# Kernel tuning notes

Measured on AMD Instinct MI355X. Metric: run time of the kernel, lower is better.

Reference implementation:

```python
import jax, jax.numpy as jnp
import numpy as np

NUM_HEADS = 16
HEAD_DIM = 64
MIN_FREQ = 1.0
MAX_FREQ = 40.0


def _rope_cos_sin(t, dtype):
    # golden_gate RoPE, pos_dim=1: geometric frequency ladder in [min_freq, max_freq],
    # positions normalized to [0,1) so max_freq ~ highest spatial frequency.
    n = HEAD_DIM // 2
    j = jnp.arange(n, dtype=dtype)
    freqs = MIN_FREQ * (MAX_FREQ / MIN_FREQ) ** (j / (n - 1))  # [n]
    pos = jnp.arange(t, dtype=dtype) / t                        # [t]
    theta = 2.0 * jnp.pi * pos[:, None] * freqs[None, :]        # [t, n]
    return jnp.cos(theta), jnp.sin(theta)


def _apply_rope(x, cos, sin):
    # x: [b, h, t, d]; rotate-half convention
    n = HEAD_DIM // 2
    x1, x2 = x[..., :n], x[..., n:]
    return jnp.concatenate([x1 * cos - x2 * sin, x1 * sin + x2 * cos], axis=-1)


def setup_inputs() -> dict:
    key = jax.random.key(0)
    ks = jax.random.split(key, 5)
    b, t, c = 4, 2048, 1024
    s = 1.0 / np.sqrt(c)
    return {
        "x": jax.random.normal(ks[0], (b, t, c), dtype=jnp.float32),
        "qkv_w": jax.random.normal(ks[1], (3 * c, c), dtype=jnp.float32) * s,
        "qkv_b": jax.random.normal(ks[2], (3 * c,), dtype=jnp.float32) * 0.01,
        "proj_w": jax.random.normal(ks[3], (c, c), dtype=jnp.float32) * s,
        "proj_b": jax.random.normal(ks[4], (c,), dtype=jnp.float32) * 0.01,
    }


def reference(x, qkv_w, qkv_b, proj_w, proj_b):
    b, t, c = x.shape
    h, d = NUM_HEADS, HEAD_DIM
    qkv = x @ qkv_w.T + qkv_b                                   # [b, t, 3c]
    qkv = qkv.reshape(b, t, 3, h, d).transpose(0, 3, 1, 2, 4)   # [b, h, t, 3, d]
    q, k, v = qkv[..., 0, :], qkv[..., 1, :], qkv[..., 2, :]    # each [b, h, t, d]
    cos, sin = _rope_cos_sin(t, x.dtype)
    q = _apply_rope(q, cos, sin)
    k = _apply_rope(k, cos, sin)
    scale = 1.0 / jnp.sqrt(jnp.asarray(d, dtype=x.dtype))
    scores = jnp.einsum("bhqd,bhkd->bhqk", q, k) * scale        # [b, h, t, t]
    attn = jax.nn.softmax(scores, axis=-1)
    out = jnp.einsum("bhqk,bhkd->bhqd", attn, v)                # [b, h, t, d]
    out = out.transpose(0, 2, 1, 3).reshape(b, t, h * d)        # [b, t, c]
    return out @ proj_w.T + proj_b
```

## Files before the change

### kernel.cpp

```cpp
#include <hip/hip_runtime.h>

typedef unsigned short u16;
typedef unsigned int   u32;
typedef __attribute__((ext_vector_type(8))) short s16x8;
typedef __attribute__((ext_vector_type(4))) float f32x4;
typedef __attribute__((ext_vector_type(16))) float f32x16;

#define MFMA16(a, b, c) __builtin_amdgcn_mfma_f32_16x16x32_bf16((a), (b), (c), 0, 0, 0)
#define MFMA32(a, b, c) __builtin_amdgcn_mfma_f32_32x32x16_bf16((a), (b), (c), 0, 0, 0)
#define EXP2R(x) __builtin_amdgcn_exp2f(x)

#define GLD16(gp, lp) __builtin_amdgcn_global_load_lds(                     \
    (const __attribute__((address_space(1))) void*)(gp),                    \
    (__attribute__((address_space(3))) void*)(lp), 16, 0, 0)

#define PWOFF 1048576ull

__device__ __forceinline__ u16 f2b(float f) {
  union { float f; unsigned i; } x; x.f = f;
  unsigned r = x.i + 0x7FFFu + ((x.i >> 16) & 1u);
  return (u16)(r >> 16);
}
__device__ __forceinline__ u32 cvtpk_bf16(float a, float b) {
  u32 r;
  asm("v_cvt_pk_bf16_f32 %0, %1, %2" : "=v"(r) : "v"(a), "v"(b));
  return r;
}
__device__ __forceinline__ s16x8 cvt8(const float* __restrict__ p) {
  f32x4 a = *(const f32x4*)p;
  f32x4 b = *(const f32x4*)(p + 4);
  union { u32 u[4]; s16x8 v; } o;
  o.u[0] = cvtpk_bf16(a[0], a[1]);
  o.u[1] = cvtpk_bf16(a[2], a[3]);
  o.u[2] = cvtpk_bf16(b[0], b[1]);
  o.u[3] = cvtpk_bf16(b[2], b[3]);
  return o.v;
}

__device__ __forceinline__ void plswap(u32& a, u32& b) {
#if __has_builtin(__builtin_amdgcn_permlane32_swap)
  auto r = __builtin_amdgcn_permlane32_swap(a, b, false, false);
  a = r[0]; b = r[1];
#else
  asm volatile("v_permlane32_swap_b32 %0, %1" : "+v"(a), "+v"(b));
#endif
}
__device__ __forceinline__ float pair32(float x, int hi) {
  union { float f; u32 u; } a, b;
  a.f = x; b.f = x;
  plswap(a.u, b.u);
  return hi ? a.f : b.f;
}
__device__ __forceinline__ s16x8 mk_pa(float e0, float e1, float e2, float e3,
                                       float e4, float e5, float e6, float e7) {
  u32 a0 = cvtpk_bf16(e0, e1), b0 = cvtpk_bf16(e4, e5);
  u32 a1 = cvtpk_bf16(e2, e3), b1 = cvtpk_bf16(e6, e7);
  plswap(a0, b0);
  plswap(a1, b1);
  union { u32 u[4]; s16x8 v; } x;
  x.u[0] = a0; x.u[1] = a1; x.u[2] = b0; x.u[3] = b1;
  return x.v;
}

#define SM_GRP(sv, ofs, pa_out, ps_out) {                                  \
    float e0 = EXP2R((sv)[(ofs) + 0] * C - mC);                            \
    float e1 = EXP2R((sv)[(ofs) + 1] * C - mC);                            \
    float e2 = EXP2R((sv)[(ofs) + 2] * C - mC);                            \
    float e3 = EXP2R((sv)[(ofs) + 3] * C - mC);                            \
    float e4 = EXP2R((sv)[(ofs) + 4] * C - mC);                            \
    float e5 = EXP2R((sv)[(ofs) + 5] * C - mC);                            \
    float e6 = EXP2R((sv)[(ofs) + 6] * C - mC);                            \
    float e7 = EXP2R((sv)[(ofs) + 7] * C - mC);                            \
    (pa_out) = mk_pa(e0, e1, e2, e3, e4, e5, e6, e7);                      \
    (ps_out) = ((e0 + e1) + (e2 + e3)) + ((e4 + e5) + (e6 + e7));          \
  }

#define QKT_P(QF, KA, KB, S0, S1) {                                        \
    _Pragma("unroll")                                                      \
    for (int r = 0; r < 16; ++r) { (S0)[r] = 0.f; (S1)[r] = 0.f; }         \
    _Pragma("unroll")                                                      \
    for (int ks = 0; ks < 4; ++ks) {                                       \
      (S0) = MFMA32((KA)[ks], (QF)[ks], (S0));                             \
      (S1) = MFMA32((KB)[ks], (QF)[ks], (S1));                             \
    }                                                                      \
  }

#define SMAX_P(S0, S1, PA0, PA1, PA2, PA3, MR, LI, O0, O1) {               \
    float m8[8];                                                           \
    _Pragma("unroll")                                                      \
    for (int r = 0; r < 8; ++r)                                            \
      m8[r] = fmaxf(fmaxf((S0)[r], (S0)[r + 8]),                           \
                    fmaxf((S1)[r], (S1)[r + 8]));                          \
    float mx = fmaxf(fmaxf(fmaxf(m8[0], m8[1]), fmaxf(m8[2], m8[3])),      \
                     fmaxf(fmaxf(m8[4], m8[5]), fmaxf(m8[6], m8[7])));     \
    mx = fmaxf(mx, pair32(mx, hi));                                        \
    if (!__all(mx - (MR) <= 8.0f)) {                                       \
      float mnew = fmaxf((MR), mx);                                        \
      float al = EXP2R(((MR) - mnew) * C);                                 \
      (MR) = mnew;                                                         \
      (LI) *= al;                                                          \
      if (hi == 0) redL[w][l31] = al;                                      \
      f32x4 a0 = *(const f32x4*)&redL[w][hi * 4];                          \
      f32x4 a1 = *(const f32x4*)&redL[w][8 + hi * 4];                      \
      f32x4 a2 = *(const f32x4*)&redL[w][16 + hi * 4];                     \
      f32x4 a3 = *(const f32x4*)&redL[w][24 + hi * 4];                     \
      _Pragma("unroll")                                                    \
      for (int e = 0; e < 4; ++e) {                                        \
        (O0)[e]      *= a0[e];  (O1)[e]      *= a0[e];                     \
        (O0)[4 + e]  *= a1[e];  (O1)[4 + e]  *= a1[e];                     \
        (O0)[8 + e]  *= a2[e];  (O1)[8 + e]  *= a2[e];                     \
        (O0)[12 + e] *= a3[e];  (O1)[12 + e] *= a3[e];                     \
      }                                                                    \
    }                                                                      \
    const float mC = (MR) * C;                                             \
    float ps0, ps1, ps2, ps3;                                              \
    SM_GRP(S0, 0, PA0, ps0);                                               \
    SM_GRP(S0, 8, PA1, ps1);                                               \
    SM_GRP(S1, 0, PA2, ps2);                                               \
    SM_GRP(S1, 8, PA3, ps3);                                               \
    float sum = (ps0 + ps1) + (ps2 + ps3);                                 \
    sum += pair32(sum, hi);                                                \
    (LI) += sum;                                                           \
  }

#define PV_P(PA0, PA1, PA2, PA3, VA, VB, O0, O1) {                         \
    (O0) = MFMA32((PA0), (VA)[0], (O0));                                   \
    (O1) = MFMA32((PA0), (VB)[0], (O1));                                   \
    (O0) = MFMA32((PA1), (VA)[1], (O0));                                   \
    (O1) = MFMA32((PA1), (VB)[1], (O1));                                   \
    (O0) = MFMA32((PA2), (VA)[2], (O0));                                   \
    (O1) = MFMA32((PA2), (VB)[2], (O1));                                   \
    (O0) = MFMA32((PA3), (VA)[3], (O0));                                   \
    (O1) = MFMA32((PA3), (VB)[3], (O1));                                   \
  }

#define ATT_EPI(LI, O0, O1, Q0) {                                          \
    if (hi == 0) redL[w][l31] = 1.0f / (LI);                               \
    f32x4 i0 = *(const f32x4*)&redL[w][hi * 4];                            \
    f32x4 i1 = *(const f32x4*)&redL[w][8 + hi * 4];                        \
    f32x4 i2 = *(const f32x4*)&redL[w][16 + hi * 4];                       \
    f32x4 i3 = *(const f32x4*)&redL[w][24 + hi * 4];                       \
    u16* Ab = AO + (size_t)p_glob * 131072 + (size_t)(Q0) * 64;            \
    _Pragma("unroll")                                                      \
    for (int g = 0; g < 4; ++g) {                                          \
      const f32x4 iv = (g == 0) ? i0 : (g == 1) ? i1 : (g == 2) ? i2 : i3; \
      _Pragma("unroll")                                                    \
      for (int e = 0; e < 4; ++e) {                                        \
        int row = g * 8 + hi * 4 + e;           \
        Ab[(size_t)row * 64 + l31]      = f2b((O0)[g * 4 + e] * iv[e]);    \
        Ab[(size_t)row * 64 + 32 + l31] = f2b((O1)[g * 4 + e] * iv[e]);    \
      }                                                                    \
    }                                                                      \
  }

__global__ void k_beacon(float* __restrict__ Out, unsigned long long ws_size) {
  float V = 3000.0f + fminf((float)(ws_size >> 20), 999.0f);
  size_t i = ((size_t)blockIdx.x * 256 + threadIdx.x) * 8;
#pragma unroll
  for (int j = 0; j < 8; ++j) Out[i + j] = V;
}

__global__ void k_convert_pw(const float* __restrict__ PW, u16* __restrict__ ws) {
  size_t i = ((size_t)blockIdx.x * 256 + threadIdx.x) * 8;
  *(s16x8*)(ws + i) = cvt8(PW + i);
}

__global__ void k_convert_xw(const float* __restrict__ X,
                             const float* __restrict__ W,
                             u16* __restrict__ dst) {
  size_t i = ((size_t)blockIdx.x * 256 + threadIdx.x) * 8;
  const float* src = (i < 8388608ull) ? (X + i) : (W + (i - 8388608ull));
  *(s16x8*)(dst + i) = cvt8(src);
}

#define QLOAD(K) {                                                 \
    la0 = *(const f32x4*)(Ag + (K));                               \
    la1 = *(const f32x4*)(Ag + (K) + 4);                           \
    lb0 = *(const f32x4*)(Ag + (size_t)64 * 1024 + (K));           \
    lb1 = *(const f32x4*)(Ag + (size_t)64 * 1024 + (K) + 4);       \
    lc0 = *(const f32x4*)(BgA + (K));                              \
    lc1 = *(const f32x4*)(BgA + (K) + 4);                          \
    ld0 = *(const f32x4*)(BgB + (K));                              \
    ld1 = *(const f32x4*)(BgB + (K) + 4);                          \
  }
#define QWRITE(BUF) {                                                         \
    union { u32 u[4]; s16x8 v; } t0, t1, t2, t3;                              \
    t0.u[0] = cvtpk_bf16(la0[0], la0[1]); t0.u[1] = cvtpk_bf16(la0[2], la0[3]); \
    t0.u[2] = cvtpk_bf16(la1[0], la1[1]); t0.u[3] = cvtpk_bf16(la1[2], la1[3]); \
    t1.u[0] = cvtpk_bf16(lb0[0], lb0[1]); t1.u[1] = cvtpk_bf16(lb0[2], lb0[3]); \
    t1.u[2] = cvtpk_bf16(lb1[0], lb1[1]); t1.u[3] = cvtpk_bf16(lb1[2], lb1[3]); \
    t2.u[0] = cvtpk_bf16(lc0[0], lc0[1]); t2.u[1] = cvtpk_bf16(lc0[2], lc0[3]); \
    t2.u[2] = cvtpk_bf16(lc1[0], lc1[1]); t2.u[3] = cvtpk_bf16(lc1[2], lc1[3]); \
    t3.u[0] = cvtpk_bf16(ld0[0], ld0[1]); t3.u[1] = cvtpk_bf16(ld0[2], ld0[3]); \
    t3.u[2] = cvtpk_bf16(ld1[0], ld1[1]); t3.u[3] = cvtpk_bf16(ld1[2], ld1[3]); \
    *(s16x8*)&(BUF)[srow * 32 + scol]               = t0.v;                   \
    *(s16x8*)&(BUF)[(srow + 64) * 32 + scol]        = t1.v;                   \
    *(s16x8*)&(BUF)[4096 + srow * 32 + scol]        = t2.v;                   \
    *(s16x8*)&(BUF)[4096 + (srow + 64) * 32 + scol] = t3.v;                   \
  }

#define QISSUEB(K, BUF) {                                          \
    GLD16(Agb + (K),          (BUF) + w * 512);                    \
    GLD16(Agb + 65536 + (K),  (BUF) + 2048 + w * 512);             \
    GLD16(BgAb + (K),         (BUF) + 4096 + w * 512);             \
    GLD16(BgBb + (K),         (BUF) + 6144 + w * 512);             \
  }

#define QKV_EPILOGUE                                                          \
  const int ncol = n0 + wc * 64;                   \
  const int which = ncol >> lgHB;                            \
  const int hh = (ncol & (HB - 1)) >> 6;                                      \
  const int cb = which * 1024 + (h0 + hh) * 64;                               \
  const int mbase = m0 + wr * 64;                                             \
  float bias[4];                                                              \
  _Pragma("unroll")                                                           \
  for (int j = 0; j < 4; ++j) bias[j] = Bias[cb + j * 16 + l16];              \
  __syncthreads();                                                            \
  u16* OSt = smem + w * 4608;                                                 \
  if (which == 2) {                                                           \
    _Pragma("unroll")                                                         \
    for (int i = 0; i < 4; ++i)                                               \
      _Pragma("unroll")                                                       \
      for (int r = 0; r < 4; ++r) {                                           \
        int tl = i * 16 + quad * 4 + r;                                       \
        _Pragma("unroll")                                                     \
        for (int j = 0; j < 4; ++j)                                           \
          OSt[(j * 16 + l16) * 72 + tl] = f2b(acc[i][j][r] + bias[j]);        \
      }                                                                       \
  } else {                                                                    \
    const float LC = 0.1716750968f;                                           \
    float fr0 = exp2f((float)l16 * LC);                                       \
    float fr1 = exp2f((float)(16 + l16) * LC);                                \
    _Pragma("unroll")                                                         \
    for (int i = 0; i < 4; ++i)                                               \
      _Pragma("unroll")                                                       \
      for (int r = 0; r < 4; ++r) {                                           \
        int tl = i * 16 + quad * 4 + r;                                       \
        int tok = mbase + tl;                                                 \
        float ps = (float)(tok & 2047) * (1.0f / 2048.0f);                    \
        float rv0 = ps * fr0; rv0 -= floorf(rv0);                             \
        float rv1 = ps * fr1; rv1 -= floorf(rv1);                             \
        float s0 = __builtin_amdgcn_sinf(rv0), c0 = __builtin_amdgcn_cosf(rv0); \
        float s1 = __builtin_amdgcn_sinf(rv1), c1 = __builtin_amdgcn_cosf(rv1); \
        float x10 = acc[i][0][r] + bias[0], x11 = acc[i][1][r] + bias[1];     \
        float x20 = acc[i][2][r] + bias[2], x21 = acc[i][3][r] + bias[3];     \
        OSt[tl * 72 + l16]      = f2b(x10 * c0 - x20 * s0);                   \
        OSt[tl * 72 + 16 + l16] = f2b(x11 * c1 - x21 * s1);                   \
        OSt[tl * 72 + 32 + l16] = f2b(x10 * s0 + x20 * c0);                   \
        OSt[tl * 72 + 48 + l16] = f2b(x11 * s1 + x21 * c1);                   \
      }                                                                       \
  }                                                                           \
  const int bb = mbase >> 11, tt0 = mbase & 2047;                             \
  const int pp = (bb << lgHG) + hh;                                           \
  if (which == 2) {                                                           \
    u16* D = Vc + ((size_t)pp * 32 + (tt0 >> 6)) * 4096;                      \
    _Pragma("unroll")                                                         \
    for (int fi = 0; fi < 8; ++fi) {                                          \
      int ks = fi >> 1, db = fi & 1;                                          \
      *(s16x8*)&D[fi * 512 + lane * 8] =                                      \
          *(const s16x8*)&OSt[(db * 32 + l31) * 72 + ks * 16 + hi * 8];       \
    }                                                                         \
  } else if (which == 1) {                                                    \
    u16* D = Kc + ((size_t)pp * 32 + (tt0 >> 6)) * 4096;                      \
    _Pragma("unroll")                                                         \
    for (int fi = 0; fi < 8; ++fi) {                                          \
      int ks = fi >> 1, kb = fi & 1;                                          \
      *(s16x8*)&D[fi * 512 + lane * 8] =                                      \
          *(const s16x8*)&OSt[(kb * 32 + l31) * 72 + ks * 16 + hi * 8];       \
    }                                                                         \
  } else {                                                                    \
    u16* D = Qc + ((size_t)pp * 64 + (tt0 >> 5)) * 2048;                      \
    _Pragma("unroll")                                                         \
    for (int fi = 0; fi < 8; ++fi) {                                          \
      int qh = fi >> 2, ks = fi & 3;                                          \
      *(s16x8*)&D[(size_t)qh * 2048 + ks * 512 + lane * 8] =                  \
          *(const s16x8*)&OSt[(qh * 32 + l31) * 72 + ks * 16 + hi * 8];       \
    }                                                                         \
  }

__global__ __launch_bounds__(256, 4) void k_qkv_rope(
    const float* __restrict__ X, const float* __restrict__ W,
    const float* __restrict__ Bias, u16* __restrict__ ws,
    int h0, int lgHB, int lgHG)
{
  __shared__ __align__(16) u16 smem[18432];

  const size_t segE = 524288ull << lgHG;
  u16* Qc = ws + PWOFF;
  u16* Kc = Qc + segE;
  u16* Vc = Kc + segE;

  const int tid = threadIdx.x;
  const int w = tid >> 6, lane = tid & 63, quad = lane >> 4, l16 = lane & 15;
  const int l31 = lane & 31, hi = lane >> 5;
  const int wr = w >> 1, wc = w & 1;
  const int HB = 1 << lgHB;

  const int gx = gridDim.x;
  const int hw = blockIdx.y * gx + blockIdx.x;
  const int cpx = (gx << 6) >> 3;
  const int lg = (hw & 7) * cpx + (hw >> 3);
  const int m0 = (lg / gx) * 128, n0 = (lg % gx) * 128;

  const f32x4 z4 = {0.f, 0.f, 0.f, 0.f};
  f32x4 acc[4][4];
#pragma unroll
  for (int i = 0; i < 4; ++i)
#pragma unroll
    for (int j = 0; j < 4; ++j) acc[i][j] = z4;

  const int srow = tid >> 2;
  const int scol = (tid & 3) * 8;
  const int nlogA = n0 + srow, nlogB = nlogA + 64;
  const int wrowA = (nlogA >> lgHB) * 1024 + (h0 + ((nlogA & (HB - 1)) >> 6)) * 64 + (nlogA & 63);
  const int wrowB = (nlogB >> lgHB) * 1024 + (h0 + ((nlogB & (HB - 1)) >> 6)) * 64 + (nlogB & 63);
  const float* Ag  = X + (size_t)(m0 + srow) * 1024 + scol;
  const float* BgA = W + (size_t)wrowA * 1024 + scol;
  const float* BgB = W + (size_t)wrowB * 1024 + scol;

  f32x4 la0, la1, lb0, lb1, lc0, lc1, ld0, ld1;
  QLOAD(0)
  QWRITE(smem)

  for (int k0 = 0; k0 < 1024; k0 += 32) {
    u16* Ac = smem + ((k0 >> 5) & 1) * 8192;
    if (k0 < 992) QLOAD(k0 + 32)
    __syncthreads();
    s16x8 af[4], bf[4];
#pragma unroll
    for (int i = 0; i < 4; ++i)
      af[i] = *(const s16x8*)&Ac[(wr * 64 + i * 16 + l16) * 32 + quad * 8];
#pragma unroll
    for (int j = 0; j < 4; ++j)
      bf[j] = *(const s16x8*)&Ac[4096 + (wc * 64 + j * 16 + l16) * 32 + quad * 8];
#pragma unroll
    for (int i = 0; i < 4; ++i)
#pragma unroll
      for (int j = 0; j < 4; ++j)
        acc[i][j] = MFMA16(af[i], bf[j], acc[i][j]);
    if (k0 < 992) {
      u16* An = smem + ((~(k0 >> 5)) & 1) * 8192;
      QWRITE(An)
    }
  }

  QKV_EPILOGUE
}

__global__ __launch_bounds__(256, 4) void k_qkv_rope_b(
    const u16* __restrict__ Xb, const u16* __restrict__ Wb,
    const float* __restrict__ Bias, u16* __restrict__ ws,
    int h0, int lgHB, int lgHG)
{
  __shared__ __align__(16) u16 smem[18432];

  const size_t segE = 524288ull << lgHG;
  u16* Qc = ws + PWOFF;
  u16* Kc = Qc + segE;
  u16* Vc = Kc + segE;

  const int tid = threadIdx.x;
  const int w = tid >> 6, lane = tid & 63, quad = lane >> 4, l16 = lane & 15;
  const int l31 = lane & 31, hi = lane >> 5;
  const int wr = w >> 1, wc = w & 1;
  const int HB = 1 << lgHB;

  const int gx = gridDim.x;
  const int hw = blockIdx.y * gx + blockIdx.x;
  const int cpx = (gx << 6) >> 3;
  const int lg = (hw & 7) * cpx + (hw >> 3);
  const int m0 = (lg / gx) * 128, n0 = (lg % gx) * 128;

  const f32x4 z4 = {0.f, 0.f, 0.f, 0.f};
  f32x4 acc[4][4];
#pragma unroll
  for (int i = 0; i < 4; ++i)
#pragma unroll
    for (int j = 0; j < 4; ++j) acc[i][j] = z4;

  const int srow = tid >> 2;
  const int scol = (tid & 3) * 8;
  const int nlogA = n0 + srow, nlogB = nlogA + 64;
  const int wrowA = (nlogA >> lgHB) * 1024 + (h0 + ((nlogA & (HB - 1)) >> 6)) * 64 + (nlogA & 63);
  const int wrowB = (nlogB >> lgHB) * 1024 + (h0 + ((nlogB & (HB - 1)) >> 6)) * 64 + (nlogB & 63);
  const u16* Agb  = Xb + (size_t)(m0 + srow) * 1024 + scol;
  const u16* BgAb = Wb + (size_t)wrowA * 1024 + scol;
  const u16* BgBb = Wb + (size_t)wrowB * 1024 + scol;

  QISSUEB(0, smem)

  for (int k0 = 0; k0 < 1024; k0 += 32) {
    u16* Ac = smem + ((k0 >> 5) & 1) * 8192;
    __syncthreads();
    if (k0 < 992) {
      u16* An = smem + ((~(k0 >> 5)) & 1) * 8192;
      QISSUEB(k0 + 32, An)
    }
    s16x8 af[4], bf[4];
#pragma unroll
    for (int i = 0; i < 4; ++i)
      af[i] = *(const s16x8*)&Ac[(wr * 64 + i * 16 + l16) * 32 + quad * 8];
#pragma unroll
    for (int j = 0; j < 4; ++j)
      bf[j] = *(const s16x8*)&Ac[4096 + (wc * 64 + j * 16 + l16) * 32 + quad * 8];
#pragma unroll
    for (int i = 0; i < 4; ++i)
#pragma unroll
      for (int j = 0; j < 4; ++j)
        acc[i][j] = MFMA16(af[i], bf[j], acc[i][j]);
  }

  QKV_EPILOGUE
}

__global__ __launch_bounds__(256, 2) void k_attn(
    u16* __restrict__ ws, u16* __restrict__ AO, int h0, int lgHG)
{
  __shared__ float redL[4][32];

  const size_t segE = 524288ull << lgHG;
  const u16* Qg = ws + PWOFF;
  const u16* Kg = Qg + segE;
  const u16* Vg = Kg + segE;

  const int tid = threadIdx.x;
  const int w = tid >> 6, lane = tid & 63;
  const int l31 = lane & 31, hi = lane >> 5;

  const int P = 4 << lgHG;
  const int n = blockIdx.y * 8 + blockIdx.x;
  const int mm = n >> 3;
  const int p  = (n & 7) * (P >> 3) + (mm >> 3);
  const int qt = mm & 7;

  const u16* Kb = Kg + (size_t)p * 131072;
  const u16* Vb = Vg + (size_t)p * 131072;
  const int q0A = qt * 256 + w * 32;
  const int q0B = q0A + 128;

  const u16* QtA = Qg + (size_t)p * 131072 + (size_t)(qt * 8 + w) * 2048;
  const u16* QtB = QtA + 4 * 2048;
  s16x8 qfA[4], qfB[4];
#pragma unroll
  for (int ks = 0; ks < 4; ++ks) {
    qfA[ks] = *(const s16x8*)&QtA[ks * 512 + lane * 8];
    qfB[ks] = *(const s16x8*)&QtB[ks * 512 + lane * 8];
  }

  f32x16 oA0, oA1, oB0, oB1;
#pragma unroll
  for (int r = 0; r < 16; ++r) { oA0[r] = 0.f; oA1[r] = 0.f; oB0[r] = 0.f; oB1[r] = 0.f; }
  float mA = -1e30f, lA = 0.f, mB = -1e30f, lB = 0.f;
  const float C = 0.1803368801f;

  for (int kt = 0; kt < 32; ++kt) {
    const u16* Kt = Kb + (size_t)kt * 4096;
    const u16* Vt = Vb + (size_t)kt * 4096;
    s16x8 kfA[4], kfB[4], vfA[4], vfB[4];
#pragma unroll
    for (int ks = 0; ks < 4; ++ks) {
      kfA[ks] = *(const s16x8*)&Kt[(ks * 2 + 0) * 512 + lane * 8];
      kfB[ks] = *(const s16x8*)&Kt[(ks * 2 + 1) * 512 + lane * 8];
    }
#pragma unroll
    for (int ks = 0; ks < 4; ++ks) {
      vfA[ks] = *(const s16x8*)&Vt[(ks * 2 + 0) * 512 + lane * 8];
      vfB[ks] = *(const s16x8*)&Vt[(ks * 2 + 1) * 512 + lane * 8];
    }

    f32x16 sA0, sA1, sB0, sB1;
    QKT_P(qfA, kfA, kfB, sA0, sA1)
    QKT_P(qfB, kfA, kfB, sB0, sB1)

    {
      s16x8 pa0, pa1, pa2, pa3;
      SMAX_P(sA0, sA1, pa0, pa1, pa2, pa3, mA, lA, oA0, oA1)
      PV_P(pa0, pa1, pa2, pa3, vfA, vfB, oA0, oA1)
    }
    {
      s16x8 pa0, pa1, pa2, pa3;
      SMAX_P(sB0, sB1, pa0, pa1, pa2, pa3, mB, lB, oB0, oB1)
      PV_P(pa0, pa1, pa2, pa3, vfA, vfB, oB0, oB1)
    }
  }

  const int p_glob = (p >> lgHG) * 16 + h0 + (p & ((1 << lgHG) - 1));
  ATT_EPI(lA, oA0, oA1, q0A)
  ATT_EPI(lB, oB0, oB1, q0B)
}

#define PISSUE(K, BUF) {                                                     \
    const int c0_ = (K) + scol;                                              \
    GLD16(Abase + (size_t)(c0_ >> 6) * 131072 + (c0_ & 63), (BUF) + w * 512); \
    GLD16(Bg + (K),          (BUF) + 2048 + w * 512);                        \
    GLD16(Bg + 65536 + (K),  (BUF) + 4096 + w * 512);                        \
  }

__global__ __launch_bounds__(256, 4) void k_proj(
    const u16* __restrict__ AO, const u16* __restrict__ W,
    const float* __restrict__ Bias, float* __restrict__ Out)
{
  __shared__ __align__(16) u16 smem[12288];

  const int tid = threadIdx.x;
  const int w = tid >> 6, lane = tid & 63, quad = lane >> 4, l16 = lane & 15;

  const int hw = blockIdx.y * 8 + blockIdx.x;
  const int lg = (hw & 7) * 128 + (hw >> 3);
  const int m0 = (lg >> 3) * 64, n0 = (lg & 7) * 128;

  const f32x4 z4 = {0.f, 0.f, 0.f, 0.f};
  f32x4 acc[4][2];
#pragma unroll
  for (int i = 0; i < 4; ++i)
#pragma unroll
    for (int j = 0; j < 2; ++j) acc[i][j] = z4;

  const int srow = tid >> 2;
  const int scol = (tid & 3) * 8;
  const int bb = m0 >> 11, tt = m0 & 2047;
  const u16* Abase = AO + (size_t)bb * 2097152 + (size_t)(tt + srow) * 64;
  const u16* Bg = W + (size_t)(n0 + srow) * 1024 + scol;

  PISSUE(0, smem)

  for (int k0 = 0; k0 < 1024; k0 += 32) {
    u16* Ac = smem + ((k0 >> 5) & 1) * 6144;
    __syncthreads();
    if (k0 < 992) {
      u16* An = smem + ((~(k0 >> 5)) & 1) * 6144;
      PISSUE(k0 + 32, An)
    }
    s16x8 af[4], bf[2];
#pragma unroll
    for (int i = 0; i < 4; ++i)
      af[i] = *(const s16x8*)&Ac[(i * 16 + l16) * 32 + quad * 8];
#pragma unroll
    for (int j = 0; j < 2; ++j)
      bf[j] = *(const s16x8*)&Ac[2048 + (w * 32 + j * 16 + l16) * 32 + quad * 8];
#pragma unroll
    for (int i = 0; i < 4; ++i)
#pragma unroll
      for (int j = 0; j < 2; ++j)
        acc[i][j] = MFMA16(af[i], bf[j], acc[i][j]);
  }

  const int ncol = n0 + w * 32;
  float bias[2];
#pragma unroll
  for (int j = 0; j < 2; ++j) bias[j] = Bias[ncol + j * 16 + l16];

  __syncthreads();
  float* OSw = (float*)smem + w * 512;
#pragma unroll
  for (int i = 0; i < 4; ++i) {
#pragma unroll
    for (int j = 0; j < 2; ++j)
#pragma unroll
      for (int r = 0; r < 4; ++r)
        OSw[(quad * 4 + r) * 32 + j * 16 + l16] = acc[i][j][r] + bias[j];
#pragma unroll
    for (int itr = 0; itr < 2; ++itr) {
      int task = itr * 64 + lane;
      int tl = task >> 3, g = task & 7;
      *(f32x4*)&Out[(size_t)(m0 + i * 16 + tl) * 1024 + ncol + g * 4] =
          *(const f32x4*)&OSw[tl * 32 + g * 4];
    }
  }
}

extern "C" void kernel_launch(void* const* d_in, const int* in_sizes, int n_in,
                              void* d_out, int out_size, void* d_ws, size_t ws_size,
                              hipStream_t stream) {
  const float* X    = (const float*)d_in[0];
  const float* QKVW = (const float*)d_in[1];
  const float* QKVB = (const float*)d_in[2];
  const float* PW   = (const float*)d_in[3];
  const float* PB   = (const float*)d_in[4];
  float* Out = (float*)d_out;
  u16* ws = (u16*)d_ws;

  int HG, lgHG, ok = 1;
  if      (ws_size >= 52428800ull) { HG = 16; lgHG = 4; }
  else if (ws_size >= 44040192ull) { HG = 8;  lgHG = 3; }
  else if (ws_size >= 31457280ull) { HG = 4;  lgHG = 2; }
  else if (ws_size >= 25165824ull) { HG = 2;  lgHG = 1; }
  else                             { HG = 2;  lgHG = 1; ok = 0; }

  if (!ok) {
    k_beacon<<<dim3(4096), 256, 0, stream>>>(Out, (unsigned long long)ws_size);
    return;
  }

  const size_t segE = 524288ull << lgHG;
  u16* Qc = ws + PWOFF;
  u16* AO = (HG == 16) ? Qc : (Qc + 3 * segE);
  const int lgHB = lgHG + 6;

  const bool fast = (HG == 16) && (ws_size >= 75497472ull);
  u16* Xb = Qc + 3 * segE;
  u16* Wb = Xb + 8388608ull;

  k_convert_pw<<<dim3(512), 256, 0, stream>>>(PW, ws);
  if (fast)
    k_convert_xw<<<dim3(5632), 256, 0, stream>>>(X, QKVW, Xb);

  const int chunks = 16 / HG;
  for (int c = 0; c < chunks; ++c) {
    int h0 = c * HG;
    if (fast)
      k_qkv_rope_b<<<dim3((3 * HG) / 2, 64), 256, 0, stream>>>(
          Xb, Wb, QKVB, ws, h0, lgHB, lgHG);
    else
      k_qkv_rope<<<dim3((3 * HG) / 2, 64), 256, 0, stream>>>(
          X, QKVW, QKVB, ws, h0, lgHB, lgHG);
    k_attn<<<dim3(8, 4 * HG), 256, 0, stream>>>(ws, AO, h0, lgHG);
  }
  k_proj<<<dim3(8, 128), 256, 0, stream>>>(AO, ws, PB, Out);
}
```

Before: 277.4 us.

## Enlarge projection GEMM tile to 128x128 and merge fp32-to-bf16 conversion launches

The output projection kernel now uses a 128x128 block tile with a 2x2 wave layout, each wave computing 64x64. This halves the grid and raises operand reuse per LDS load, at the cost of more accumulator registers and LDS per block. Separately, the projection-weight conversion is folded into the X/QKV-weight conversion kernel, which removes one launch on the fast path.

```diff
diff --git a/kernel.cpp b/kernel.cpp
--- a/kernel.cpp
+++ b/kernel.cpp
@@ -165,12 +165,18 @@
   *(s16x8*)(ws + i) = cvt8(PW + i);
 }
 
-__global__ void k_convert_xw(const float* __restrict__ X,
-                             const float* __restrict__ W,
-                             u16* __restrict__ dst) {
+__global__ void k_convert_all(const float* __restrict__ PW,
+                              const float* __restrict__ X,
+                              const float* __restrict__ W,
+                              u16* __restrict__ ws, u16* __restrict__ Xb) {
   size_t i = ((size_t)blockIdx.x * 256 + threadIdx.x) * 8;
-  const float* src = (i < 8388608ull) ? (X + i) : (W + (i - 8388608ull));
-  *(s16x8*)(dst + i) = cvt8(src);
+  if (i < 1048576ull) {
+    *(s16x8*)(ws + i) = cvt8(PW + i);
+  } else {
+    size_t j = i - 1048576ull;
+    const float* src = (j < 8388608ull) ? (X + j) : (W + (j - 8388608ull));
+    *(s16x8*)(Xb + j) = cvt8(src);
+  }
 }
 
 #define QLOAD(K) {                                                 \
@@ -491,30 +497,33 @@
 
 #define PISSUE(K, BUF) {                                                     \
     const int c0_ = (K) + scol;                                              \
-    GLD16(Abase + (size_t)(c0_ >> 6) * 131072 + (c0_ & 63), (BUF) + w * 512); \
-    GLD16(Bg + (K),          (BUF) + 2048 + w * 512);                        \
-    GLD16(Bg + 65536 + (K),  (BUF) + 4096 + w * 512);                        \
+    const size_t aoff_ = (size_t)(c0_ >> 6) * 131072 + (c0_ & 63);           \
+    GLD16(Abase + aoff_,         (BUF) + w * 512);                           \
+    GLD16(Abase + 4096 + aoff_,  (BUF) + 2048 + w * 512);                    \
+    GLD16(Bg + (K),              (BUF) + 4096 + w * 512);                    \
+    GLD16(Bg + 65536 + (K),      (BUF) + 6144 + w * 512);                    \
   }
 
 __global__ __launch_bounds__(256, 4) void k_proj(
     const u16* __restrict__ AO, const u16* __restrict__ W,
     const float* __restrict__ Bias, float* __restrict__ Out)
 {
-  __shared__ __align__(16) u16 smem[12288];
+  __shared__ __align__(16) u16 smem[16384];
 
   const int tid = threadIdx.x;
   const int w = tid >> 6, lane = tid & 63, quad = lane >> 4, l16 = lane & 15;
+  const int wr = w >> 1, wc = w & 1;
 
   const int hw = blockIdx.y * 8 + blockIdx.x;
-  const int lg = (hw & 7) * 128 + (hw >> 3);
-  const int m0 = (lg >> 3) * 64, n0 = (lg & 7) * 128;
+  const int lg = (hw & 7) * 64 + (hw >> 3);
+  const int m0 = (lg >> 3) * 128, n0 = (lg & 7) * 128;
 
   const f32x4 z4 = {0.f, 0.f, 0.f, 0.f};
-  f32x4 acc[4][2];
+  f32x4 acc[4][4];
 #pragma unroll
   for (int i = 0; i < 4; ++i)
 #pragma unroll
-    for (int j = 0; j < 2; ++j) acc[i][j] = z4;
+    for (int j = 0; j < 4; ++j) acc[i][j] = z4;
 
   const int srow = tid >> 2;
   const int scol = (tid & 3) * 8;
@@ -525,46 +534,53 @@
   PISSUE(0, smem)
 
   for (int k0 = 0; k0 < 1024; k0 += 32) {
-    u16* Ac = smem + ((k0 >> 5) & 1) * 6144;
+    u16* Ac = smem + ((k0 >> 5) & 1) * 8192;
     __syncthreads();
     if (k0 < 992) {
-      u16* An = smem + ((~(k0 >> 5)) & 1) * 6144;
+      u16* An = smem + ((~(k0 >> 5)) & 1) * 8192;
       PISSUE(k0 + 32, An)
     }
-    s16x8 af[4], bf[2];
+    s16x8 af[4], bf[4];
 #pragma unroll
     for (int i = 0; i < 4; ++i)
-      af[i] = *(const s16x8*)&Ac[(i * 16 + l16) * 32 + quad * 8];
-#pragma unroll
-    for (int j = 0; j < 2; ++j)
-      bf[j] = *(const s16x8*)&Ac[2048 + (w * 32 + j * 16 + l16) * 32 + quad * 8];
+      af[i] = *(const s16x8*)&Ac[(wr * 64 + i * 16 + l16) * 32 + quad * 8];
+#pragma unroll
+    for (int j = 0; j < 4; ++j)
+      bf[j] = *(const s16x8*)&Ac[4096 + (wc * 64 + j * 16 + l16) * 32 + quad * 8];
 #pragma unroll
     for (int i = 0; i < 4; ++i)
 #pragma unroll
-      for (int j = 0; j < 2; ++j)
+      for (int j = 0; j < 4; ++j)
         acc[i][j] = MFMA16(af[i], bf[j], acc[i][j]);
   }
 
-  const int ncol = n0 + w * 32;
-  float bias[2];
-#pragma unroll
-  for (int j = 0; j < 2; ++j) bias[j] = Bias[ncol + j * 16 + l16];
+  const int ncol = n0 + wc * 64;
+  float bias[4];
+#pragma unroll
+  for (int j = 0; j < 4; ++j) bias[j] = Bias[ncol + j * 16 + l16];
 
   __syncthreads();
-  float* OSw = (float*)smem + w * 512;
-#pragma unroll
-  for (int i = 0; i < 4; ++i) {
-#pragma unroll
-    for (int j = 0; j < 2; ++j)
-#pragma unroll
-      for (int r = 0; r < 4; ++r)
-        OSw[(quad * 4 + r) * 32 + j * 16 + l16] = acc[i][j][r] + bias[j];
-#pragma unroll
-    for (int itr = 0; itr < 2; ++itr) {
+  float* OSw = (float*)smem + w * 2048;
+#pragma unroll
+  for (int h = 0; h < 2; ++h) {
+#pragma unroll
+    for (int ii = 0; ii < 2; ++ii) {
+      int i = h * 2 + ii;
+#pragma unroll
+      for (int j = 0; j < 4; ++j)
+#pragma unroll
+        for (int r = 0; r < 4; ++r) {
+          int tl = ii * 16 + quad * 4 + r;
+          OSw[tl * 64 + j * 16 + l16] = acc[i][j][r] + bias[j];
+        }
+    }
+#pragma unroll
+    for (int itr = 0; itr < 8; ++itr) {
       int task = itr * 64 + lane;
-      int tl = task >> 3, g = task & 7;
-      *(f32x4*)&Out[(size_t)(m0 + i * 16 + tl) * 1024 + ncol + g * 4] =
-          *(const f32x4*)&OSw[tl * 32 + g * 4];
+      int tl = task >> 4, g = task & 15;
+      int row = m0 + wr * 64 + h * 32 + tl;
+      *(f32x4*)&Out[(size_t)row * 1024 + ncol + g * 4] =
+          *(const f32x4*)&OSw[tl * 64 + g * 4];
     }
   }
 }
@@ -601,9 +617,10 @@
   u16* Xb = Qc + 3 * segE;
   u16* Wb = Xb + 8388608ull;
 
-  k_convert_pw<<<dim3(512), 256, 0, stream>>>(PW, ws);
   if (fast)
-    k_convert_xw<<<dim3(5632), 256, 0, stream>>>(X, QKVW, Xb);
+    k_convert_all<<<dim3(6144), 256, 0, stream>>>(PW, X, QKVW, ws, Xb);
+  else
+    k_convert_pw<<<dim3(512), 256, 0, stream>>>(PW, ws);
 
   const int chunks = 16 / HG;
   for (int c = 0; c < chunks; ++c) {
@@ -616,5 +633,5 @@
           X, QKVW, QKVB, ws, h0, lgHB, lgHG);
     k_attn<<<dim3(8, 4 * HG), 256, 0, stream>>>(ws, AO, h0, lgHG);
   }
-  k_proj<<<dim3(8, 128), 256, 0, stream>>>(AO, ws, PB, Out);
-}
+  k_proj<<<dim3(8, 64), 256, 0, stream>>>(AO, ws, PB, Out);
+}
```

After: 274.8 us. No clear change (-0.9%).
